# Kernel optimization log

Measured on AMD Instinct MI355X. Metric: run time of the kernel, lower is better.

Reference implementation:

```python
import jax, jax.numpy as jnp
import numpy as np

NUM_HEADS = 8

def setup_inputs() -> dict:
    key0 = jax.random.key(0)
    ks = jax.random.split(key0, 6)
    T, S, B, E = 2048, 2048, 2, 256
    W_SCALE = 0.06  # ~xavier_uniform std for 256x256
    return {
        "query": jax.random.normal(ks[0], (T, B, E), dtype=jnp.float32),
        "key": jax.random.normal(ks[1], (S, B, E), dtype=jnp.float32),
        "value": jax.random.normal(ks[2], (S, B, E), dtype=jnp.float32),
        "Wq": jax.random.normal(ks[3], (E, E), dtype=jnp.float32) * W_SCALE,
        "bq": jnp.zeros((E,), dtype=jnp.float32),
        "Wk": jax.random.normal(ks[4], (E, E), dtype=jnp.float32) * W_SCALE,
        "bk": jnp.zeros((E,), dtype=jnp.float32),
        "Wo": jax.random.normal(ks[5], (E, E), dtype=jnp.float32) * W_SCALE,
        "bo": jnp.zeros((E,), dtype=jnp.float32),
    }

def reference(query, key, value, Wq, bq, Wk, bk, Wo, bo):
    # query: [T,B,E], key/value: [S,B,E]
    T, B, E = query.shape
    S = key.shape[0]
    H = NUM_HEADS
    Dh = E // H
    q = jnp.einsum('tbe,fe->tbf', query, Wq) + bq
    k = jnp.einsum('sbe,fe->sbf', key, Wk) + bk
    # split heads: view(L, B*H, Dh) == reshape(L, B, H, Dh)
    qh = q.reshape(T, B, H, Dh)
    kh = k.reshape(S, B, H, Dh)
    vh = value.reshape(S, B, H, Dh)  # v is NOT projected in this module
    scale = 1.0 / jnp.sqrt(jnp.asarray(Dh, dtype=query.dtype))
    scores = jnp.einsum('tbhd,sbhd->bhts', qh * scale, kh)  # [B,H,T,S]
    attn = jax.nn.softmax(scores, axis=-1)
    out = jnp.einsum('bhts,sbhd->tbhd', attn, vh).reshape(T, B, E)
    # residual output projection: out + linear(out)
    out = out + jnp.einsum('tbe,fe->tbf', out, Wo) + bo
    avg_weights = jnp.mean(attn, axis=1)  # [B,T,S]
    return (out, avg_weights)
```

## Files before the change

kernel.cpp:

```cpp
#include <hip/hip_runtime.h>
#include <hip/hip_fp16.h>

#define T_DIM 2048
#define S_DIM 2048
#define B_DIM 2
#define E_DIM 256
#define H_DIM 8
#define DH 32

typedef _Float16 half8 __attribute__((ext_vector_type(8)));
typedef _Float16 half4 __attribute__((ext_vector_type(4)));
typedef float floatx4 __attribute__((ext_vector_type(4)));

#if defined(__has_builtin)
#if __has_builtin(__builtin_amdgcn_exp2f)
#define EXPFN(x) __builtin_amdgcn_exp2f(x)
#define LOG2E_FOLD 1.4426950408889634f
#endif
#endif
#ifndef EXPFN
#define EXPFN(x) __expf(x)
#define LOG2E_FOLD 1.0f
#endif

#define XS 264

__global__ __launch_bounds__(256, 4) void k1_proj_vt(
    const float* __restrict__ Q, const float* __restrict__ K,
    const float* __restrict__ V,
    const float* __restrict__ Wq, const float* __restrict__ Wk,
    const float* __restrict__ bq, const float* __restrict__ bk,
    _Float16* __restrict__ Qp, _Float16* __restrict__ Kp,
    _Float16* __restrict__ Vt2, float scale_q) {
  __shared__ __align__(16) _Float16 smem[64 * XS];
  int tid = threadIdx.x;
  int bx = blockIdx.x;
  if (bx < 512) {
    int z = bx >> 8;
    int rem = bx & 255;
    int r0 = (rem >> 2) * 64;
    int c0 = (rem & 3) * 64;
    const float* X = z ? K : Q;
    const float* W = z ? Wk : Wq;
    const float* bias = z ? bk : bq;
    _Float16* outp = z ? Kp : Qp;
    float scale = z ? 1.0f : scale_q;
    _Float16* Xs = smem;
    int lane = tid & 63, w = tid >> 6;
    int quad = lane >> 4, l16 = lane & 15;
#pragma unroll
    for (int it = 0; it < 16; ++it) {
      int row = (tid >> 6) + it * 4, col = (tid & 63) * 4;
      float4 a = *(const float4*)(X + (size_t)(r0 + row) * 256 + col);
      half4 hx;
      hx[0] = (_Float16)a.x; hx[1] = (_Float16)a.y;
      hx[2] = (_Float16)a.z; hx[3] = (_Float16)a.w;
      *(half4*)(Xs + row * XS + col) = hx;
    }
    __syncthreads();

    floatx4 c[4] = {{0.f,0.f,0.f,0.f},{0.f,0.f,0.f,0.f},{0.f,0.f,0.f,0.f},{0.f,0.f,0.f,0.f}};
    int arow = w * 16 + l16;
    const float* Wr0 = W + (size_t)(c0 + l16) * 256 + quad * 8;
#pragma unroll 2
    for (int k0 = 0; k0 < 256; k0 += 32) {
      half8 af = *(const half8*)(Xs + arow * XS + k0 + quad * 8);
#pragma unroll
      for (int j = 0; j < 4; ++j) {
        const float* Wr = Wr0 + j * 16 * 256 + k0;
        float4 w0 = *(const float4*)(Wr);
        float4 w1 = *(const float4*)(Wr + 4);
        half8 bf;
        bf[0] = (_Float16)w0.x; bf[1] = (_Float16)w0.y;
        bf[2] = (_Float16)w0.z; bf[3] = (_Float16)w0.w;
        bf[4] = (_Float16)w1.x; bf[5] = (_Float16)w1.y;
        bf[6] = (_Float16)w1.z; bf[7] = (_Float16)w1.w;
        c[j] = __builtin_amdgcn_mfma_f32_16x16x32_f16(af, bf, c[j], 0, 0, 0);
      }
    }
#pragma unroll
    for (int j = 0; j < 4; ++j) {
      int f = c0 + j * 16 + l16;
      float bv = bias[f];
      int h = f >> 5, d = f & 31;
#pragma unroll
      for (int r = 0; r < 4; ++r) {
        int row = r0 + w * 16 + quad * 4 + r;
        int t = row >> 1, b = row & 1;
        outp[(((size_t)b * H_DIM + h) * T_DIM + t) * DH + d] =
            (_Float16)((c[j][r] + bv) * scale);
      }
    }
  } else {
    float (*tile)[33] = (float (*)[33])smem;
    int b2 = bx - 512;
    int st = b2 & 31, h = (b2 >> 5) & 7, b = b2 >> 8;
    int s0 = st * 64;
    int d = tid & 31, sr = tid >> 5;
#pragma unroll
    for (int k = 0; k < 8; ++k) {
      int s = sr + k * 8;
      tile[s][d] = V[((size_t)(s0 + s) * B_DIM + b) * E_DIM + h * DH + d];
    }
    __syncthreads();
    int si = tid & 63, dq = tid >> 6;
    size_t base = ((size_t)b * H_DIM + h) * 128 * 512;
    int tl = st * 4 + (si >> 4);
    int sl = si & 15;
#pragma unroll
    for (int m = 0; m < 8; ++m) {
      int dd = dq * 8 + m;
      Vt2[base + (size_t)tl * 512 + dd * 16 + sl] = (_Float16)tile[si][dd];
    }
  }
}

#define OSTRIDE 36

#define ATTN_STEP(cur, nxt, PRE)                                                \
  {                                                                             \
    if (PRE) {                                                                  \
      kf[nxt] = *(const half8*)kp;                                              \
      v0[nxt] = *(const half4*)vp;                                              \
      v1[nxt] = *(const half4*)(vp + 256);                                      \
      kp += 512; vp += 512;                                                     \
    }                                                                           \
    _Pragma("unroll")                                                           \
    for (int j = 0; j < 4; ++j) {                                               \
      floatx4 c = {0.f, 0.f, 0.f, 0.f};                                         \
      c = __builtin_amdgcn_mfma_f32_16x16x32_f16(kf[cur], qf[j], c, 0, 0, 0);   \
      float e0 = EXPFN(c[0]), e1 = EXPFN(c[1]), e2 = EXPFN(c[2]), e3 = EXPFN(c[3]); \
      ls[j] += (e0 + e1) + (e2 + e3);                                           \
      half4 p;                                                                  \
      p[0] = (_Float16)e0; p[1] = (_Float16)e1;                                 \
      p[2] = (_Float16)e2; p[3] = (_Float16)e3;                                 \
      o[j][0] = __builtin_amdgcn_mfma_f32_16x16x16f16(p, v0[cur], o[j][0], 0, 0, 0); \
      o[j][1] = __builtin_amdgcn_mfma_f32_16x16x16f16(p, v1[cur], o[j][1], 0, 0, 0); \
    }                                                                           \
  }

__global__ __launch_bounds__(512, 4) void attn_o_kernel(const _Float16* __restrict__ Qp,
                                                        const _Float16* __restrict__ Kp,
                                                        const _Float16* __restrict__ Vt2,
                                                        _Float16* __restrict__ Of16,
                                                        float* __restrict__ lsum) {
  __shared__ float stageO[8][64 * OSTRIDE];
  __shared__ float lstage[8][64];

  int tid = threadIdx.x;
  int lane = tid & 63, w = tid >> 6;
  int quad = lane >> 4, l16 = lane & 15;
  int bx = blockIdx.x;
  int h = bx & 7, b = (bx >> 3) & 1, tcc = bx >> 4;
  int t0 = tcc << 6;

  const _Float16* Qb = Qp + (((size_t)b * H_DIM + h) * T_DIM + t0) * DH;

  half8 qf[4];
#pragma unroll
  for (int j = 0; j < 4; ++j)
    qf[j] = *(const half8*)(Qb + (size_t)(j * 16 + l16) * DH + quad * 8);

  floatx4 o[4][2];
#pragma unroll
  for (int j = 0; j < 4; ++j) { o[j][0] = (floatx4){0,0,0,0}; o[j][1] = (floatx4){0,0,0,0}; }
  float ls[4] = {0.f, 0.f, 0.f, 0.f};

  int tile0 = w * 16;
  const _Float16* kp = Kp + ((size_t)b * H_DIM + h) * S_DIM * DH +
                       (size_t)(tile0 * 16 + l16) * DH + quad * 8;
  const _Float16* vp = Vt2 + ((size_t)b * H_DIM + h) * 128 * 512 +
                       (size_t)tile0 * 512 + l16 * 16 + quad * 4;

  half8 kf[2];
  half4 v0[2], v1[2];
  kf[0] = *(const half8*)kp;
  v0[0] = *(const half4*)vp;
  v1[0] = *(const half4*)(vp + 256);
  kp += 512; vp += 512;

  for (int ii = 0; ii < 7; ++ii) {
    ATTN_STEP(0, 1, true);
    ATTN_STEP(1, 0, true);
  }
  ATTN_STEP(0, 1, true);
  ATTN_STEP(1, 0, false);

#pragma unroll
  for (int j = 0; j < 4; ++j) {
    float v = ls[j];
    v += __shfl_xor(v, 16, 64);
    v += __shfl_xor(v, 32, 64);
    if (quad == 0) lstage[w][j * 16 + l16] = v;
  }
#pragma unroll
  for (int j = 0; j < 4; ++j)
#pragma unroll
    for (int r = 0; r < 4; ++r) {
      stageO[w][(j * 16 + quad * 4 + r) * OSTRIDE + l16] = o[j][0][r];
      stageO[w][(j * 16 + quad * 4 + r) * OSTRIDE + 16 + l16] = o[j][1][r];
    }
  __syncthreads();

  int t = tid >> 3, d0 = (tid & 7) * 4;
  floatx4 os = {0.f, 0.f, 0.f, 0.f};
  float lr = 0.f;
#pragma unroll
  for (int ww = 0; ww < 8; ++ww) {
    os += *(const floatx4*)&stageO[ww][t * OSTRIDE + d0];
    lr += lstage[ww][t];
  }
  float rl = 1.0f / lr;
  half4 oh;
  oh[0] = (_Float16)(os[0] * rl); oh[1] = (_Float16)(os[1] * rl);
  oh[2] = (_Float16)(os[2] * rl); oh[3] = (_Float16)(os[3] * rl);
  *(half4*)(Of16 + ((size_t)(t0 + t) * B_DIM + b) * E_DIM + h * DH + d0) = oh;
  if (tid < 64) {
    float s = 0.f;
#pragma unroll
    for (int ww = 0; ww < 8; ++ww) s += lstage[ww][tid];
    lsum[((size_t)b * H_DIM + h) * T_DIM + t0 + tid] = s;
  }
}

#define ASTRIDE 132
__global__ __launch_bounds__(512, 4) void k3_avg_outproj(
    const _Float16* __restrict__ Qp, const _Float16* __restrict__ Kp,
    const float* __restrict__ lsum, const _Float16* __restrict__ Of16,
    const float* __restrict__ Wo, const float* __restrict__ bo,
    float* __restrict__ avg_out, float* __restrict__ out) {
  __shared__ __align__(16) float smem[128 * ASTRIDE];
  int tid = threadIdx.x;
  int lane = tid & 63, w = tid >> 6;
  int quad = lane >> 4, l16 = lane & 15;
  int bx = blockIdx.x;

  if (bx < 512) {
    int sc = bx & 15, tc = (bx >> 4) & 15, b = bx >> 8;
    int t0 = tc * 128, s0 = sc * 128;
    int tw = t0 + w * 16;

    floatx4 acc[8];
#pragma unroll
    for (int st = 0; st < 8; ++st) acc[st] = (floatx4){0.f, 0.f, 0.f, 0.f};

    const _Float16* qp = Qp + (size_t)b * H_DIM * T_DIM * DH +
                         (size_t)(tw + l16) * DH + quad * 8;
    const _Float16* kp = Kp + (size_t)b * H_DIM * S_DIM * DH +
                         (size_t)(s0 + l16) * DH + quad * 8;
    const float* lp = lsum + (size_t)b * H_DIM * T_DIM + tw + l16;

    for (int h = 0; h < H_DIM; ++h) {
      half8 qfrag = *(const half8*)qp;
      float rlv = 0.125f / *lp;
#pragma unroll
      for (int st = 0; st < 8; ++st) {
        half8 kfr = *(const half8*)(kp + st * 512);
        floatx4 c = {0.f, 0.f, 0.f, 0.f};
        c = __builtin_amdgcn_mfma_f32_16x16x32_f16(kfr, qfrag, c, 0, 0, 0);
#pragma unroll
        for (int r = 0; r < 4; ++r) acc[st][r] += EXPFN(c[r]) * rlv;
      }
      qp += (size_t)T_DIM * DH;
      kp += (size_t)S_DIM * DH;
      lp += T_DIM;
    }
#pragma unroll
    for (int st = 0; st < 8; ++st)
      *(floatx4*)&smem[(w * 16 + l16) * ASTRIDE + st * 16 + quad * 4] = acc[st];
    __syncthreads();

    int rbase = tid >> 4, seg = tid & 15;
#pragma unroll
    for (int rr = 0; rr < 4; ++rr) {
      int row = rr * 32 + rbase;
      const float* srcl = &smem[row * ASTRIDE];
      float* dst = avg_out + ((size_t)b * T_DIM + t0 + row) * S_DIM + s0;
#pragma unroll
      for (int k = 0; k < 2; ++k) {
        int col = seg * 4 + k * 64;
        *(floatx4*)(dst + col) = *(const floatx4*)(srcl + col);
      }
    }
  } else {
    int bo_ = bx - 512;
    int r0 = (bo_ >> 2) * 128;
    int c0 = (bo_ & 3) * 64;
    _Float16* Ws = (_Float16*)smem;
#pragma unroll
    for (int it = 0; it < 8; ++it) {
      int row = (tid >> 6) + it * 8, col = (tid & 63) * 4;
      int f = c0 + row;
      float4 a = *(const float4*)(Wo + (size_t)f * 256 + col);
      half4 hv;
      hv[0] = (_Float16)a.x; hv[1] = (_Float16)a.y;
      hv[2] = (_Float16)a.z; hv[3] = (_Float16)a.w;
      int di = f - col;
      if (di >= 0 && di < 4) hv[di] += (_Float16)1.0f;
      *(half4*)(Ws + row * XS + col) = hv;
    }
    __syncthreads();

    floatx4 c[4] = {{0.f,0.f,0.f,0.f},{0.f,0.f,0.f,0.f},{0.f,0.f,0.f,0.f},{0.f,0.f,0.f,0.f}};
    int grow = r0 + w * 16 + l16;
#pragma unroll 2
    for (int k0 = 0; k0 < 256; k0 += 32) {
      half8 af = *(const half8*)(Of16 + (size_t)grow * 256 + k0 + quad * 8);
#pragma unroll
      for (int j = 0; j < 4; ++j) {
        half8 bf = *(const half8*)(Ws + (j * 16 + l16) * XS + k0 + quad * 8);
        c[j] = __builtin_amdgcn_mfma_f32_16x16x32_f16(af, bf, c[j], 0, 0, 0);
      }
    }
#pragma unroll
    for (int j = 0; j < 4; ++j) {
      int f = c0 + j * 16 + l16;
      float bv = bo[f];
#pragma unroll
      for (int r = 0; r < 4; ++r) {
        int row = r0 + w * 16 + quad * 4 + r;
        out[(size_t)row * 256 + f] = c[j][r] + bv;
      }
    }
  }
}

extern "C" void kernel_launch(void* const* d_in, const int* in_sizes, int n_in,
                              void* d_out, int out_size, void* d_ws, size_t ws_size,
                              hipStream_t stream) {
  const float* query = (const float*)d_in[0];
  const float* key   = (const float*)d_in[1];
  const float* value = (const float*)d_in[2];
  const float* Wq    = (const float*)d_in[3];
  const float* bq    = (const float*)d_in[4];
  const float* Wk    = (const float*)d_in[5];
  const float* bk    = (const float*)d_in[6];
  const float* Wo    = (const float*)d_in[7];
  const float* bo    = (const float*)d_in[8];

  float* out = (float*)d_out;
  float* avg_out = out + (size_t)T_DIM * B_DIM * E_DIM;

  char* ws = (char*)d_ws;
  _Float16* Qp   = (_Float16*)ws;
  _Float16* Kp   = (_Float16*)(ws + (2u << 20));
  _Float16* Vt2  = (_Float16*)(ws + (4u << 20));
  _Float16* Of16 = (_Float16*)(ws + (6u << 20));
  float*    lsum = (float*)(ws + (8u << 20));

  const float scale_q = 0.17677669529663687f * LOG2E_FOLD;

  k1_proj_vt<<<dim3(1024), dim3(256), 0, stream>>>(query, key, value, Wq, Wk,
                                                   bq, bk, Qp, Kp, Vt2, scale_q);
  attn_o_kernel<<<dim3(512), dim3(512), 0, stream>>>(Qp, Kp, Vt2, Of16, lsum);
  k3_avg_outproj<<<dim3(640), dim3(512), 0, stream>>>(Qp, Kp, lsum, Of16, Wo, bo,
                                                      avg_out, out);
}
```

Before: 140.9 us.

## Fuse three kernels into one cooperative persistent kernel with grid syncs

Replaces the three separate launches (projection/V transpose, attention, avg-weights plus output projection) with a single cooperative kernel of 256 blocks that loops over the work units of each phase and separates phases with grid.sync(). This removes launch gaps and tail effects between kernels. In exchange, occupancy is capped at one 512-thread block per CU with large shared memory and fewer blocks, so each phase runs with less parallelism. The old three-kernel path stays as a fallback if the cooperative launch fails, and launch bounds on those kernels were lowered to 2.

```diff
diff --git a/kernel.cpp b/kernel.cpp
--- a/kernel.cpp
+++ b/kernel.cpp
@@ -1,5 +1,8 @@
 #include <hip/hip_runtime.h>
 #include <hip/hip_fp16.h>
+#include <hip/hip_cooperative_groups.h>
+
+namespace cg = cooperative_groups;
 
 #define T_DIM 2048
 #define S_DIM 2048
@@ -24,6 +27,317 @@
 #endif
 
 #define XS 264
+#define OSTRIDE 36
+#define ASTRIDE 132
+
+#define ATTN_STEP(cur, nxt, PRE)                                                \
+  {                                                                             \
+    if (PRE) {                                                                  \
+      kf[nxt] = *(const half8*)kp;                                              \
+      v0[nxt] = *(const half4*)vp;                                              \
+      v1[nxt] = *(const half4*)(vp + 256);                                      \
+      kp += 512; vp += 512;                                                     \
+    }                                                                           \
+    _Pragma("unroll")                                                           \
+    for (int j = 0; j < 4; ++j) {                                               \
+      floatx4 c = {0.f, 0.f, 0.f, 0.f};                                         \
+      c = __builtin_amdgcn_mfma_f32_16x16x32_f16(kf[cur], qf[j], c, 0, 0, 0);   \
+      float e0 = EXPFN(c[0]), e1 = EXPFN(c[1]), e2 = EXPFN(c[2]), e3 = EXPFN(c[3]); \
+      ls[j] += (e0 + e1) + (e2 + e3);                                           \
+      half4 p;                                                                  \
+      p[0] = (_Float16)e0; p[1] = (_Float16)e1;                                 \
+      p[2] = (_Float16)e2; p[3] = (_Float16)e3;                                 \
+      o[j][0] = __builtin_amdgcn_mfma_f32_16x16x16f16(p, v0[cur], o[j][0], 0, 0, 0); \
+      o[j][1] = __builtin_amdgcn_mfma_f32_16x16x16f16(p, v1[cur], o[j][1], 0, 0, 0); \
+    }                                                                           \
+  }
+
+__global__ __launch_bounds__(512, 2) void fused_all(
+    const float* __restrict__ Q, const float* __restrict__ K,
+    const float* __restrict__ V,
+    const float* __restrict__ Wq, const float* __restrict__ Wk,
+    const float* __restrict__ bq, const float* __restrict__ bk,
+    const float* __restrict__ Wo, const float* __restrict__ bo,
+    _Float16* __restrict__ Qp, _Float16* __restrict__ Kp,
+    _Float16* __restrict__ Vt2, _Float16* __restrict__ Of16,
+    float* __restrict__ lsum, float* __restrict__ out,
+    float* __restrict__ avg_out, float scale_q) {
+  __shared__ __align__(16) char smem_raw[75776];
+  cg::grid_group grid = cg::this_grid();
+  int tid = threadIdx.x;
+  int bx = blockIdx.x;
+
+  {
+    int tid2 = tid & 255;
+    int half = tid >> 8;
+    _Float16* hs = (_Float16*)(smem_raw + half * 33792);
+    for (int uu = 0; uu < 2; ++uu) {
+      int u = bx * 4 + half * 2 + uu;
+      if (u < 512) {
+        int z = u >> 8;
+        int rem = u & 255;
+        int r0 = (rem >> 2) * 64;
+        const float* X = z ? K : Q;
+#pragma unroll
+        for (int it = 0; it < 16; ++it) {
+          int row = (tid2 >> 6) + it * 4, col = (tid2 & 63) * 4;
+          float4 a = *(const float4*)(X + (size_t)(r0 + row) * 256 + col);
+          half4 hx;
+          hx[0] = (_Float16)a.x; hx[1] = (_Float16)a.y;
+          hx[2] = (_Float16)a.z; hx[3] = (_Float16)a.w;
+          *(half4*)(hs + row * XS + col) = hx;
+        }
+      } else {
+        float (*tile)[33] = (float (*)[33])hs;
+        int b2 = u - 512;
+        int st = b2 & 31, h = (b2 >> 5) & 7, b = b2 >> 8;
+        int s0 = st * 64;
+        int d = tid2 & 31, sr = tid2 >> 5;
+#pragma unroll
+        for (int k = 0; k < 8; ++k) {
+          int s = sr + k * 8;
+          tile[s][d] = V[((size_t)(s0 + s) * B_DIM + b) * E_DIM + h * DH + d];
+        }
+      }
+      __syncthreads();
+      if (u < 512) {
+        int z = u >> 8;
+        int rem = u & 255;
+        int r0 = (rem >> 2) * 64;
+        int c0 = (rem & 3) * 64;
+        const float* W = z ? Wk : Wq;
+        const float* bias = z ? bk : bq;
+        _Float16* outp = z ? Kp : Qp;
+        float scale = z ? 1.0f : scale_q;
+        int lane = tid2 & 63, w4 = tid2 >> 6;
+        int quad = lane >> 4, l16 = lane & 15;
+        floatx4 c[4] = {{0.f,0.f,0.f,0.f},{0.f,0.f,0.f,0.f},{0.f,0.f,0.f,0.f},{0.f,0.f,0.f,0.f}};
+        int arow = w4 * 16 + l16;
+        const float* Wr0 = W + (size_t)(c0 + l16) * 256 + quad * 8;
+#pragma unroll 2
+        for (int k0 = 0; k0 < 256; k0 += 32) {
+          half8 af = *(const half8*)(hs + arow * XS + k0 + quad * 8);
+#pragma unroll
+          for (int j = 0; j < 4; ++j) {
+            const float* Wr = Wr0 + j * 16 * 256 + k0;
+            float4 w0 = *(const float4*)(Wr);
+            float4 w1 = *(const float4*)(Wr + 4);
+            half8 bf;
+            bf[0] = (_Float16)w0.x; bf[1] = (_Float16)w0.y;
+            bf[2] = (_Float16)w0.z; bf[3] = (_Float16)w0.w;
+            bf[4] = (_Float16)w1.x; bf[5] = (_Float16)w1.y;
+            bf[6] = (_Float16)w1.z; bf[7] = (_Float16)w1.w;
+            c[j] = __builtin_amdgcn_mfma_f32_16x16x32_f16(af, bf, c[j], 0, 0, 0);
+          }
+        }
+#pragma unroll
+        for (int j = 0; j < 4; ++j) {
+          int f = c0 + j * 16 + l16;
+          float bv = bias[f];
+          int h = f >> 5, d = f & 31;
+#pragma unroll
+          for (int r = 0; r < 4; ++r) {
+            int row = r0 + w4 * 16 + quad * 4 + r;
+            int t = row >> 1, b = row & 1;
+            outp[(((size_t)b * H_DIM + h) * T_DIM + t) * DH + d] =
+                (_Float16)((c[j][r] + bv) * scale);
+          }
+        }
+      } else {
+        float (*tile)[33] = (float (*)[33])hs;
+        int b2 = u - 512;
+        int st = b2 & 31, h = (b2 >> 5) & 7, b = b2 >> 8;
+        int si = tid2 & 63, dq = tid2 >> 6;
+        size_t base = ((size_t)b * H_DIM + h) * 128 * 512;
+        int tl = st * 4 + (si >> 4);
+        int sl = si & 15;
+#pragma unroll
+        for (int m = 0; m < 8; ++m) {
+          int dd = dq * 8 + m;
+          Vt2[base + (size_t)tl * 512 + dd * 16 + sl] = (_Float16)tile[si][dd];
+        }
+      }
+      __syncthreads();
+    }
+  }
+  grid.sync();
+
+  {
+    float* stageO = (float*)smem_raw;
+    float* lstage = (float*)(smem_raw + 73728);
+    int lane = tid & 63, w = tid >> 6;
+    int quad = lane >> 4, l16 = lane & 15;
+    int h = bx & 7, b = (bx >> 3) & 1;
+    const _Float16* KbBase = Kp + ((size_t)b * H_DIM + h) * S_DIM * DH;
+    const _Float16* VbBase = Vt2 + ((size_t)b * H_DIM + h) * 128 * 512;
+    for (int rep = 0; rep < 2; ++rep) {
+      int t0 = (((bx >> 4) << 1) + rep) << 6;
+      const _Float16* Qb = Qp + (((size_t)b * H_DIM + h) * T_DIM + t0) * DH;
+
+      half8 qf[4];
+#pragma unroll
+      for (int j = 0; j < 4; ++j)
+        qf[j] = *(const half8*)(Qb + (size_t)(j * 16 + l16) * DH + quad * 8);
+
+      floatx4 o[4][2];
+#pragma unroll
+      for (int j = 0; j < 4; ++j) { o[j][0] = (floatx4){0,0,0,0}; o[j][1] = (floatx4){0,0,0,0}; }
+      float ls[4] = {0.f, 0.f, 0.f, 0.f};
+
+      int tile0 = w * 16;
+      const _Float16* kp = KbBase + (size_t)(tile0 * 16 + l16) * DH + quad * 8;
+      const _Float16* vp = VbBase + (size_t)tile0 * 512 + l16 * 16 + quad * 4;
+
+      half8 kf[2];
+      half4 v0[2], v1[2];
+      kf[0] = *(const half8*)kp;
+      v0[0] = *(const half4*)vp;
+      v1[0] = *(const half4*)(vp + 256);
+      kp += 512; vp += 512;
+
+      for (int ii = 0; ii < 7; ++ii) {
+        ATTN_STEP(0, 1, true);
+        ATTN_STEP(1, 0, true);
+      }
+      ATTN_STEP(0, 1, true);
+      ATTN_STEP(1, 0, false);
+
+#pragma unroll
+      for (int j = 0; j < 4; ++j) {
+        float v = ls[j];
+        v += __shfl_xor(v, 16, 64);
+        v += __shfl_xor(v, 32, 64);
+        if (quad == 0) lstage[w * 64 + j * 16 + l16] = v;
+      }
+#pragma unroll
+      for (int j = 0; j < 4; ++j)
+#pragma unroll
+        for (int r = 0; r < 4; ++r) {
+          stageO[w * 2304 + (j * 16 + quad * 4 + r) * OSTRIDE + l16] = o[j][0][r];
+          stageO[w * 2304 + (j * 16 + quad * 4 + r) * OSTRIDE + 16 + l16] = o[j][1][r];
+        }
+      __syncthreads();
+
+      int t = tid >> 3, d0 = (tid & 7) * 4;
+      floatx4 os = {0.f, 0.f, 0.f, 0.f};
+      float lr = 0.f;
+#pragma unroll
+      for (int ww = 0; ww < 8; ++ww) {
+        os += *(const floatx4*)&stageO[ww * 2304 + t * OSTRIDE + d0];
+        lr += lstage[ww * 64 + t];
+      }
+      float rl = 1.0f / lr;
+      half4 oh;
+      oh[0] = (_Float16)(os[0] * rl); oh[1] = (_Float16)(os[1] * rl);
+      oh[2] = (_Float16)(os[2] * rl); oh[3] = (_Float16)(os[3] * rl);
+      *(half4*)(Of16 + ((size_t)(t0 + t) * B_DIM + b) * E_DIM + h * DH + d0) = oh;
+      if (tid < 64) {
+        float s = 0.f;
+#pragma unroll
+        for (int ww = 0; ww < 8; ++ww) s += lstage[ww * 64 + tid];
+        lsum[((size_t)b * H_DIM + h) * T_DIM + t0 + tid] = s;
+      }
+      __syncthreads();
+    }
+  }
+  grid.sync();
+
+  {
+    float* smemf = (float*)smem_raw;
+    int lane = tid & 63, w = tid >> 6;
+    int quad = lane >> 4, l16 = lane & 15;
+    for (int rep = 0; rep < 2; ++rep) {
+      int u = bx * 2 + rep;
+      int sc = u & 15, tc = (u >> 4) & 15, b = u >> 8;
+      int t0 = tc * 128, s0 = sc * 128;
+      int tw = t0 + w * 16;
+
+      floatx4 acc[8];
+#pragma unroll
+      for (int st = 0; st < 8; ++st) acc[st] = (floatx4){0.f, 0.f, 0.f, 0.f};
+
+      const _Float16* qp = Qp + (size_t)b * H_DIM * T_DIM * DH +
+                           (size_t)(tw + l16) * DH + quad * 8;
+      const _Float16* kp = Kp + (size_t)b * H_DIM * S_DIM * DH +
+                           (size_t)(s0 + l16) * DH + quad * 8;
+      const float* lp = lsum + (size_t)b * H_DIM * T_DIM + tw + l16;
+
+      for (int h = 0; h < H_DIM; ++h) {
+        half8 qfrag = *(const half8*)qp;
+        float rlv = 0.125f / *lp;
+#pragma unroll
+        for (int st = 0; st < 8; ++st) {
+          half8 kfr = *(const half8*)(kp + st * 512);
+          floatx4 c = {0.f, 0.f, 0.f, 0.f};
+          c = __builtin_amdgcn_mfma_f32_16x16x32_f16(kfr, qfrag, c, 0, 0, 0);
+#pragma unroll
+          for (int r = 0; r < 4; ++r) acc[st][r] += EXPFN(c[r]) * rlv;
+        }
+        qp += (size_t)T_DIM * DH;
+        kp += (size_t)S_DIM * DH;
+        lp += T_DIM;
+      }
+#pragma unroll
+      for (int st = 0; st < 8; ++st)
+        *(floatx4*)&smemf[(w * 16 + l16) * ASTRIDE + st * 16 + quad * 4] = acc[st];
+      __syncthreads();
+
+      int rbase = tid >> 4, seg = tid & 15;
+#pragma unroll
+      for (int rr = 0; rr < 4; ++rr) {
+        int row = rr * 32 + rbase;
+        const float* srcl = &smemf[row * ASTRIDE];
+        float* dst = avg_out + ((size_t)b * T_DIM + t0 + row) * S_DIM + s0;
+#pragma unroll
+        for (int k = 0; k < 2; ++k) {
+          int col = seg * 4 + k * 64;
+          *(floatx4*)(dst + col) = *(const floatx4*)(srcl + col);
+        }
+      }
+      __syncthreads();
+    }
+
+    int r0o = (bx >> 2) * 64, c0o = (bx & 3) * 64;
+    _Float16* Ws = (_Float16*)smem_raw;
+#pragma unroll
+    for (int it = 0; it < 8; ++it) {
+      int row = (tid >> 6) + it * 8, col = (tid & 63) * 4;
+      int f = c0o + row;
+      float4 a = *(const float4*)(Wo + (size_t)f * 256 + col);
+      half4 hv;
+      hv[0] = (_Float16)a.x; hv[1] = (_Float16)a.y;
+      hv[2] = (_Float16)a.z; hv[3] = (_Float16)a.w;
+      int di = f - col;
+      if (di >= 0 && di < 4) hv[di] += (_Float16)1.0f;
+      *(half4*)(Ws + row * XS + col) = hv;
+    }
+    __syncthreads();
+
+    int rsel = w & 3, csel = w >> 2;
+    floatx4 c0acc = {0.f, 0.f, 0.f, 0.f};
+    floatx4 c1acc = {0.f, 0.f, 0.f, 0.f};
+    int grow = r0o + rsel * 16 + l16;
+    const _Float16* Arow = Of16 + (size_t)grow * 256 + quad * 8;
+    const _Float16* Wsrow0 = Ws + (size_t)(csel * 32 + l16) * XS + quad * 8;
+    const _Float16* Wsrow1 = Wsrow0 + 16 * XS;
+#pragma unroll 2
+    for (int k0 = 0; k0 < 256; k0 += 32) {
+      half8 af = *(const half8*)(Arow + k0);
+      half8 bf0 = *(const half8*)(Wsrow0 + k0);
+      half8 bf1 = *(const half8*)(Wsrow1 + k0);
+      c0acc = __builtin_amdgcn_mfma_f32_16x16x32_f16(af, bf0, c0acc, 0, 0, 0);
+      c1acc = __builtin_amdgcn_mfma_f32_16x16x32_f16(af, bf1, c1acc, 0, 0, 0);
+    }
+    int f0 = c0o + csel * 32 + l16;
+    float bv0 = bo[f0], bv1 = bo[f0 + 16];
+#pragma unroll
+    for (int r = 0; r < 4; ++r) {
+      int row = r0o + rsel * 16 + quad * 4 + r;
+      out[(size_t)row * 256 + f0] = c0acc[r] + bv0;
+      out[(size_t)row * 256 + f0 + 16] = c1acc[r] + bv1;
+    }
+  }
+}
 
 __global__ __launch_bounds__(256, 4) void k1_proj_vt(
     const float* __restrict__ Q, const float* __restrict__ K,
@@ -58,7 +372,6 @@
       *(half4*)(Xs + row * XS + col) = hx;
     }
     __syncthreads();
-
     floatx4 c[4] = {{0.f,0.f,0.f,0.f},{0.f,0.f,0.f,0.f},{0.f,0.f,0.f,0.f},{0.f,0.f,0.f,0.f}};
     int arow = w * 16 + l16;
     const float* Wr0 = W + (size_t)(c0 + l16) * 256 + quad * 8;
@@ -115,77 +428,45 @@
   }
 }
 
-#define OSTRIDE 36
-
-#define ATTN_STEP(cur, nxt, PRE)                                                \
-  {                                                                             \
-    if (PRE) {                                                                  \
-      kf[nxt] = *(const half8*)kp;                                              \
-      v0[nxt] = *(const half4*)vp;                                              \
-      v1[nxt] = *(const half4*)(vp + 256);                                      \
-      kp += 512; vp += 512;                                                     \
-    }                                                                           \
-    _Pragma("unroll")                                                           \
-    for (int j = 0; j < 4; ++j) {                                               \
-      floatx4 c = {0.f, 0.f, 0.f, 0.f};                                         \
-      c = __builtin_amdgcn_mfma_f32_16x16x32_f16(kf[cur], qf[j], c, 0, 0, 0);   \
-      float e0 = EXPFN(c[0]), e1 = EXPFN(c[1]), e2 = EXPFN(c[2]), e3 = EXPFN(c[3]); \
-      ls[j] += (e0 + e1) + (e2 + e3);                                           \
-      half4 p;                                                                  \
-      p[0] = (_Float16)e0; p[1] = (_Float16)e1;                                 \
-      p[2] = (_Float16)e2; p[3] = (_Float16)e3;                                 \
-      o[j][0] = __builtin_amdgcn_mfma_f32_16x16x16f16(p, v0[cur], o[j][0], 0, 0, 0); \
-      o[j][1] = __builtin_amdgcn_mfma_f32_16x16x16f16(p, v1[cur], o[j][1], 0, 0, 0); \
-    }                                                                           \
-  }
-
-__global__ __launch_bounds__(512, 4) void attn_o_kernel(const _Float16* __restrict__ Qp,
+__global__ __launch_bounds__(512, 2) void attn_o_kernel(const _Float16* __restrict__ Qp,
                                                         const _Float16* __restrict__ Kp,
                                                         const _Float16* __restrict__ Vt2,
                                                         _Float16* __restrict__ Of16,
                                                         float* __restrict__ lsum) {
   __shared__ float stageO[8][64 * OSTRIDE];
   __shared__ float lstage[8][64];
-
   int tid = threadIdx.x;
   int lane = tid & 63, w = tid >> 6;
   int quad = lane >> 4, l16 = lane & 15;
   int bx = blockIdx.x;
   int h = bx & 7, b = (bx >> 3) & 1, tcc = bx >> 4;
   int t0 = tcc << 6;
-
   const _Float16* Qb = Qp + (((size_t)b * H_DIM + h) * T_DIM + t0) * DH;
-
   half8 qf[4];
 #pragma unroll
   for (int j = 0; j < 4; ++j)
     qf[j] = *(const half8*)(Qb + (size_t)(j * 16 + l16) * DH + quad * 8);
-
   floatx4 o[4][2];
 #pragma unroll
   for (int j = 0; j < 4; ++j) { o[j][0] = (floatx4){0,0,0,0}; o[j][1] = (floatx4){0,0,0,0}; }
   float ls[4] = {0.f, 0.f, 0.f, 0.f};
-
   int tile0 = w * 16;
   const _Float16* kp = Kp + ((size_t)b * H_DIM + h) * S_DIM * DH +
                        (size_t)(tile0 * 16 + l16) * DH + quad * 8;
   const _Float16* vp = Vt2 + ((size_t)b * H_DIM + h) * 128 * 512 +
                        (size_t)tile0 * 512 + l16 * 16 + quad * 4;
-
   half8 kf[2];
   half4 v0[2], v1[2];
   kf[0] = *(const half8*)kp;
   v0[0] = *(const half4*)vp;
   v1[0] = *(const half4*)(vp + 256);
   kp += 512; vp += 512;
-
   for (int ii = 0; ii < 7; ++ii) {
     ATTN_STEP(0, 1, true);
     ATTN_STEP(1, 0, true);
   }
   ATTN_STEP(0, 1, true);
   ATTN_STEP(1, 0, false);
-
 #pragma unroll
   for (int j = 0; j < 4; ++j) {
     float v = ls[j];
@@ -201,7 +482,6 @@
       stageO[w][(j * 16 + quad * 4 + r) * OSTRIDE + 16 + l16] = o[j][1][r];
     }
   __syncthreads();
-
   int t = tid >> 3, d0 = (tid & 7) * 4;
   floatx4 os = {0.f, 0.f, 0.f, 0.f};
   float lr = 0.f;
@@ -223,8 +503,7 @@
   }
 }
 
-#define ASTRIDE 132
-__global__ __launch_bounds__(512, 4) void k3_avg_outproj(
+__global__ __launch_bounds__(512, 2) void k3_avg_outproj(
     const _Float16* __restrict__ Qp, const _Float16* __restrict__ Kp,
     const float* __restrict__ lsum, const _Float16* __restrict__ Of16,
     const float* __restrict__ Wo, const float* __restrict__ bo,
@@ -234,22 +513,18 @@
   int lane = tid & 63, w = tid >> 6;
   int quad = lane >> 4, l16 = lane & 15;
   int bx = blockIdx.x;
-
   if (bx < 512) {
     int sc = bx & 15, tc = (bx >> 4) & 15, b = bx >> 8;
     int t0 = tc * 128, s0 = sc * 128;
     int tw = t0 + w * 16;
-
     floatx4 acc[8];
 #pragma unroll
     for (int st = 0; st < 8; ++st) acc[st] = (floatx4){0.f, 0.f, 0.f, 0.f};
-
     const _Float16* qp = Qp + (size_t)b * H_DIM * T_DIM * DH +
                          (size_t)(tw + l16) * DH + quad * 8;
     const _Float16* kp = Kp + (size_t)b * H_DIM * S_DIM * DH +
                          (size_t)(s0 + l16) * DH + quad * 8;
     const float* lp = lsum + (size_t)b * H_DIM * T_DIM + tw + l16;
-
     for (int h = 0; h < H_DIM; ++h) {
       half8 qfrag = *(const half8*)qp;
       float rlv = 0.125f / *lp;
@@ -269,7 +544,6 @@
     for (int st = 0; st < 8; ++st)
       *(floatx4*)&smem[(w * 16 + l16) * ASTRIDE + st * 16 + quad * 4] = acc[st];
     __syncthreads();
-
     int rbase = tid >> 4, seg = tid & 15;
 #pragma unroll
     for (int rr = 0; rr < 4; ++rr) {
@@ -300,7 +574,6 @@
       *(half4*)(Ws + row * XS + col) = hv;
     }
     __syncthreads();
-
     floatx4 c[4] = {{0.f,0.f,0.f,0.f},{0.f,0.f,0.f,0.f},{0.f,0.f,0.f,0.f},{0.f,0.f,0.f,0.f}};
     int grow = r0 + w * 16 + l16;
 #pragma unroll 2
@@ -348,11 +621,21 @@
   _Float16* Of16 = (_Float16*)(ws + (6u << 20));
   float*    lsum = (float*)(ws + (8u << 20));
 
-  const float scale_q = 0.17677669529663687f * LOG2E_FOLD;
-
-  k1_proj_vt<<<dim3(1024), dim3(256), 0, stream>>>(query, key, value, Wq, Wk,
-                                                   bq, bk, Qp, Kp, Vt2, scale_q);
-  attn_o_kernel<<<dim3(512), dim3(512), 0, stream>>>(Qp, Kp, Vt2, Of16, lsum);
-  k3_avg_outproj<<<dim3(640), dim3(512), 0, stream>>>(Qp, Kp, lsum, Of16, Wo, bo,
-                                                      avg_out, out);
+  float scale_q = 0.17677669529663687f * LOG2E_FOLD;
+
+  void* kargs[] = {(void*)&query, (void*)&key, (void*)&value,
+                   (void*)&Wq, (void*)&Wk, (void*)&bq, (void*)&bk,
+                   (void*)&Wo, (void*)&bo,
+                   (void*)&Qp, (void*)&Kp, (void*)&Vt2, (void*)&Of16,
+                   (void*)&lsum, (void*)&out, (void*)&avg_out,
+                   (void*)&scale_q};
+  hipError_t err = hipLaunchCooperativeKernel((const void*)fused_all, dim3(256),
+                                              dim3(512), kargs, 0, stream);
+  if (err != hipSuccess) {
+    k1_proj_vt<<<dim3(1024), dim3(256), 0, stream>>>(query, key, value, Wq, Wk,
+                                                     bq, bk, Qp, Kp, Vt2, scale_q);
+    attn_o_kernel<<<dim3(512), dim3(512), 0, stream>>>(Qp, Kp, Vt2, Of16, lsum);
+    k3_avg_outproj<<<dim3(640), dim3(512), 0, stream>>>(Qp, Kp, lsum, Of16, Wo, bo,
+                                                        avg_out, out);
+  }
 }
```

New measurement: 236.5 us. +67.9%, slower.
